# Kernel optimization log

Hardware: AMD Instinct MI355X
Metric: run time of the kernel (lower is better)

The kernel has to match this reference:

```python
import jax, jax.numpy as jnp
import numpy as np

AUX_LOSS_ALPHA = 0.01
TOP_K = 2
N_EXPERTS = 64


def setup_inputs() -> dict:
    key = jax.random.key(0)
    k1, k2 = jax.random.split(key)
    B, S, H, E = 4, 4096, 2048, N_EXPERTS
    hidden_states = jax.random.normal(k1, (B, S, H), dtype=jnp.float32)
    # kaiming_uniform_(a=sqrt(5)) ~ U(-1/sqrt(H), 1/sqrt(H))
    bound = 1.0 / np.sqrt(H)
    weight = jax.random.uniform(k2, (E, H), dtype=jnp.float32, minval=-bound, maxval=bound)
    return {"hidden_states": hidden_states, "weight": weight}


def reference(hidden_states, weight):
    B, S, H = hidden_states.shape
    E, K = N_EXPERTS, TOP_K
    x = hidden_states.reshape(-1, H)              # [T, H], T = B*S
    logits = jnp.einsum('th,eh->te', x, weight)   # router GEMM [T, E]
    scores = jax.nn.softmax(logits, axis=-1)
    topk_weight, topk_idx = jax.lax.top_k(scores, K)  # [T, K]
    # norm_topk_prob (K > 1)
    topk_weight = topk_weight / (jnp.sum(topk_weight, axis=-1, keepdims=True) + 1e-20)
    # seq_aux auxiliary loss (training path)
    idx2d = topk_idx.reshape(B, S * K)            # [B, S*K]
    ce = jnp.zeros((B, E), dtype=scores.dtype)
    ce = ce.at[jnp.arange(B)[:, None], idx2d].add(1.0)
    ce = ce / (S * K / E)
    scores3 = scores.reshape(B, S, E)
    aux_loss = jnp.mean(jnp.sum(ce * jnp.mean(scores3, axis=1), axis=1)) * AUX_LOSS_ALPHA
    return topk_idx, topk_weight, aux_loss
```

## Files before the change

kernel.cpp:

```cpp
#include <hip/hip_runtime.h>
#include <math.h>


#define TT 16384
#define HH 2048
#define EE 64
#define BB 4
#define M_TOK 16
#define KCH 256
#define TAU 2e-3f
#define NREP 8

typedef float v4f __attribute__((ext_vector_type(4)));
typedef float f4v __attribute__((ext_vector_type(4)));
typedef short s8v __attribute__((ext_vector_type(8)));

__device__ __forceinline__ unsigned short f2bf(float f) {
    unsigned u = __float_as_uint(f);
    return (unsigned short)((u + 0x7fffu + ((u >> 16) & 1u)) >> 16);
}
__device__ __forceinline__ float bf2f(unsigned short h) {
    return __uint_as_float(((unsigned)h) << 16);
}

__global__ void prep_b(const float* __restrict__ w,
                       unsigned short* __restrict__ bhi,
                       unsigned short* __restrict__ blo) {
    int idx = blockIdx.x * blockDim.x + threadIdx.x;
    int j    = idx & 7;
    int lane = (idx >> 3) & 63;
    int ks   = (idx >> 9) & 63;
    int nt   = idx >> 15;
    int e = nt * 16 + (lane & 15);
    int k = ks * 32 + (lane >> 4) * 8 + j;
    float f = w[e * HH + k];
    unsigned short h = f2bf(f);
    bhi[idx] = h;
    blo[idx] = f2bf(f - bf2f(h));
}

__global__ __launch_bounds__(256) void gemm_logits(
    const float* __restrict__ x,
    const unsigned short* __restrict__ bhi, const unsigned short* __restrict__ blo,
    float* __restrict__ logits) {

    __shared__ unsigned short ahi[2][8 * 64 * 8];
    __shared__ unsigned short alo[2][8 * 64 * 8];

    const int tid  = threadIdx.x;
    const int wave = tid >> 6;
    const int lane = tid & 63;
    const int tok0 = blockIdx.x * M_TOK;
    const int m  = tid >> 4;
    const int kb = tid & 15;

    v4f rx[2][4];

    auto LD = [&](int c, int s) {
        const float* __restrict__ xp = x + (size_t)(tok0 + m) * HH + c * KCH + kb * 8;
        rx[s][0] = *(const v4f*)xp;
        rx[s][1] = *(const v4f*)(xp + 4);
        rx[s][2] = *(const v4f*)(xp + 128);
        rx[s][3] = *(const v4f*)(xp + 132);
    };
    auto ST = [&](int s, int bi) {
#pragma unroll
        for (int g = 0; g < 2; ++g) {
            v4f a = rx[s][g * 2], b2 = rx[s][g * 2 + 1];
            float xs[8] = {a.x, a.y, a.z, a.w, b2.x, b2.y, b2.z, b2.w};
            s8v hv, lv;
#pragma unroll
            for (int j = 0; j < 8; ++j) {
                unsigned short h = f2bf(xs[j]);
                hv[j] = (short)h;
                lv[j] = (short)f2bf(xs[j] - bf2f(h));
            }
            const int k8i = kb + g * 16;
            const int kstep = k8i >> 2, quad = k8i & 3;
            const int entry = kstep * 64 + quad * 16 + (m ^ (quad << 1));
            *(s8v*)&ahi[bi][entry * 8] = hv;
            *(s8v*)&alo[bi][entry * 8] = lv;
        }
    };

    LD(0, 0);
    LD(1, 1);
    ST(0, 0);
    __syncthreads();

    f4v acc = {0.f, 0.f, 0.f, 0.f};
    const int rdl = lane ^ ((lane >> 4) << 1);

#pragma unroll
    for (int c = 0; c < 8; ++c) {
        const int cur = c & 1;
        if (c < 6) LD(c + 2, cur);
        if (c < 7) ST(cur ^ 1, cur ^ 1);
#pragma unroll
        for (int ks = 0; ks < 8; ++ks) {
            const int entry = ks * 64 + rdl;
            s8v af_h = *(const s8v*)&ahi[cur][entry * 8];
            s8v af_l = *(const s8v*)&alo[cur][entry * 8];
            const size_t boff = ((size_t)(wave * 64 + c * 8 + ks) * 64 + lane) * 8;
            s8v bf_h = *(const s8v*)&bhi[boff];
            s8v bf_l = *(const s8v*)&blo[boff];
            acc = __builtin_amdgcn_mfma_f32_16x16x32_bf16(af_h, bf_h, acc, 0, 0, 0);
            acc = __builtin_amdgcn_mfma_f32_16x16x32_bf16(af_h, bf_l, acc, 0, 0, 0);
            acc = __builtin_amdgcn_mfma_f32_16x16x32_bf16(af_l, bf_h, acc, 0, 0, 0);
        }
        __syncthreads();
    }

#pragma unroll
    for (int r = 0; r < 4; ++r)
        logits[(size_t)(tok0 + (lane >> 4) * 4 + r) * EE + wave * 16 + (lane & 15)] = acc[r];
}

__global__ __launch_bounds__(256) void gate_topk(
    const float* __restrict__ logits,
    float* __restrict__ out_idx, float* __restrict__ out_w,
    float* __restrict__ g_cnt, float* __restrict__ g_ssum,
    int* __restrict__ wl_cnt, int* __restrict__ wl) {

    __shared__ float bssum[EE];
    const int tid  = threadIdx.x;
    const int lane = tid & 63;
    const int t    = blockIdx.x * 4 + (tid >> 6);
    const int rep  = (blockIdx.x & (NREP - 1)) * (BB * EE);

    if (tid < EE) bssum[tid] = 0.f;

    float l = logits[(size_t)t * EE + lane];

    float mx = l;
#pragma unroll
    for (int off = 32; off; off >>= 1) mx = fmaxf(mx, __shfl_xor(mx, off, 64));
    float p = __expf(l - mx);
    float Z = p;
#pragma unroll
    for (int off = 32; off; off >>= 1) Z += __shfl_xor(Z, off, 64);
    float s = p / Z;

    float v = l;
    int cand[4]; float cl[4];
#pragma unroll
    for (int r = 0; r < 4; ++r) {
        float bv = v; int bi = lane;
#pragma unroll
        for (int off = 32; off; off >>= 1) {
            float ov = __shfl_xor(bv, off, 64);
            int   oi = __shfl_xor(bi, off, 64);
            if (ov > bv || (ov == bv && oi < bi)) { bv = ov; bi = oi; }
        }
        cand[r] = bi; cl[r] = bv;
        if (lane == bi) v = -3.4e38f;
    }

    __syncthreads();
    atomicAdd(&bssum[lane], s);

    if (lane == 0) {
        const int b = t >> 12;
        atomicAdd(&g_cnt[rep + b * EE + cand[0]], 1.f);
        atomicAdd(&g_cnt[rep + b * EE + cand[1]], 1.f);
        float w1 = 1.f / (1.f + __expf(cl[1] - cl[0]));
        out_idx[t * 2]     = (float)cand[0];
        out_idx[t * 2 + 1] = (float)cand[1];
        out_w[t * 2]       = w1;
        out_w[t * 2 + 1]   = 1.f - w1;
        if (cl[0] - cl[1] < TAU || cl[1] - cl[2] < TAU) {
            int pos = atomicAdd(wl_cnt, 1);
            wl[pos] = t;
        }
    }

    __syncthreads();
    if (tid < EE) {
        const int b0 = (blockIdx.x * 4) >> 12;
        atomicAdd(&g_ssum[rep + b0 * EE + tid], bssum[tid]);
    }
}

__global__ __launch_bounds__(256) void rerank_exact(
    const float* __restrict__ logits, const float* __restrict__ x,
    const float* __restrict__ w,
    const int* __restrict__ wl_cnt, const int* __restrict__ wl,
    float* __restrict__ out_idx, float* __restrict__ out_w) {

    const int lane = threadIdx.x & 63;
    const int wid  = blockIdx.x * 4 + (threadIdx.x >> 6);
    const int n    = wl_cnt[0];

    for (int i = wid; i < n; i += 32 * 4) {
        const int t = wl[i];
        float l = logits[(size_t)t * EE + lane];

        float v = l;
        int cand[4];
#pragma unroll
        for (int r = 0; r < 4; ++r) {
            float bv = v; int bi = lane;
#pragma unroll
            for (int off = 32; off; off >>= 1) {
                float ov = __shfl_xor(bv, off, 64);
                int   oi = __shfl_xor(bi, off, 64);
                if (ov > bv || (ov == bv && oi < bi)) { bv = ov; bi = oi; }
            }
            cand[r] = bi;
            if (lane == bi) v = -3.4e38f;
        }

        const float* __restrict__ xt  = x + (size_t)t * HH;
        const float* __restrict__ w0p = w + (size_t)cand[0] * HH;
        const float* __restrict__ w1p = w + (size_t)cand[1] * HH;
        const float* __restrict__ w2p = w + (size_t)cand[2] * HH;
        const float* __restrict__ w3p = w + (size_t)cand[3] * HH;
        double d0 = 0.0, d1 = 0.0, d2 = 0.0, d3 = 0.0;
#pragma unroll
        for (int ii = 0; ii < 8; ++ii) {
            const int k = ii * 256 + lane * 4;
            v4f xv = *(const v4f*)(xt + k);
            v4f a0 = *(const v4f*)(w0p + k);
            v4f a1 = *(const v4f*)(w1p + k);
            v4f a2 = *(const v4f*)(w2p + k);
            v4f a3 = *(const v4f*)(w3p + k);
            double dx0 = (double)xv.x, dx1 = (double)xv.y;
            double dx2 = (double)xv.z, dx3 = (double)xv.w;
            d0 = fma(dx0, (double)a0.x, d0); d0 = fma(dx1, (double)a0.y, d0);
            d0 = fma(dx2, (double)a0.z, d0); d0 = fma(dx3, (double)a0.w, d0);
            d1 = fma(dx0, (double)a1.x, d1); d1 = fma(dx1, (double)a1.y, d1);
            d1 = fma(dx2, (double)a1.z, d1); d1 = fma(dx3, (double)a1.w, d1);
            d2 = fma(dx0, (double)a2.x, d2); d2 = fma(dx1, (double)a2.y, d2);
            d2 = fma(dx2, (double)a2.z, d2); d2 = fma(dx3, (double)a2.w, d2);
            d3 = fma(dx0, (double)a3.x, d3); d3 = fma(dx1, (double)a3.y, d3);
            d3 = fma(dx2, (double)a3.z, d3); d3 = fma(dx3, (double)a3.w, d3);
        }
#pragma unroll
        for (int off = 32; off; off >>= 1) {
            d0 += __shfl_xor(d0, off, 64);
            d1 += __shfl_xor(d1, off, 64);
            d2 += __shfl_xor(d2, off, 64);
            d3 += __shfl_xor(d3, off, 64);
        }

        double bd[4] = {d0, d1, d2, d3};
        int e1 = cand[0]; double l1 = bd[0];
#pragma unroll
        for (int r = 1; r < 4; ++r)
            if (bd[r] > l1 || (bd[r] == l1 && cand[r] < e1)) { l1 = bd[r]; e1 = cand[r]; }
        int e2 = -1; double l2 = -1e300;
#pragma unroll
        for (int r = 0; r < 4; ++r) {
            if (cand[r] == e1) continue;
            if (e2 < 0 || bd[r] > l2 || (bd[r] == l2 && cand[r] < e2)) { l2 = bd[r]; e2 = cand[r]; }
        }

        double w1 = 1.0 / (1.0 + exp(l2 - l1));
        if (lane == 0) {
            out_idx[t * 2]     = (float)e1;
            out_idx[t * 2 + 1] = (float)e2;
            out_w[t * 2]       = (float)w1;
            out_w[t * 2 + 1]   = (float)(1.0 - w1);
        }
    }
}

__global__ void finalize(const float* __restrict__ g_cnt,
                         const float* __restrict__ g_ssum,
                         float* __restrict__ aux_out) {
    int lane = threadIdx.x;
    float a = 0.f;
    for (int b = 0; b < BB; ++b) {
        float c = 0.f, ss = 0.f;
#pragma unroll
        for (int r = 0; r < NREP; ++r) {
            c  += g_cnt[r * (BB * EE) + b * EE + lane];
            ss += g_ssum[r * (BB * EE) + b * EE + lane];
        }
        a += c * ss;
    }
#pragma unroll
    for (int off = 32; off; off >>= 1) a += __shfl_xor(a, off, 64);
    if (lane == 0) aux_out[0] = a * (0.01f / (4.f * 128.f * 4096.f));
}

extern "C" void kernel_launch(void* const* d_in, const int* in_sizes, int n_in,
                              void* d_out, int out_size, void* d_ws, size_t ws_size,
                              hipStream_t stream) {
    const float* x = (const float*)d_in[0];
    const float* w = (const float*)d_in[1];
    float* out = (float*)d_out;
    float* out_idx = out;
    float* out_w   = out + 2 * TT;
    float* aux     = out + 4 * TT;

    float* logits = (float*)d_ws;
    unsigned short* bhi = (unsigned short*)(logits + (size_t)TT * EE);
    unsigned short* blo = bhi + (size_t)EE * HH;
    float* g_cnt  = (float*)(blo + (size_t)EE * HH);
    float* g_ssum = g_cnt + NREP * BB * EE;
    int*   wl_cnt = (int*)(g_ssum + NREP * BB * EE);
    int*   wl     = wl_cnt + 16;

    hipMemsetAsync(g_cnt, 0, (2 * NREP * BB * EE + 16) * sizeof(float), stream);
    prep_b<<<(EE * HH) / 256, 256, 0, stream>>>(w, bhi, blo);
    gemm_logits<<<TT / M_TOK, 256, 0, stream>>>(x, bhi, blo, logits);
    gate_topk<<<TT / 4, 256, 0, stream>>>(logits, out_idx, out_w,
                                          g_cnt, g_ssum, wl_cnt, wl);
    rerank_exact<<<32, 256, 0, stream>>>(logits, x, w, wl_cnt, wl, out_idx, out_w);
    finalize<<<1, 64, 0, stream>>>(g_cnt, g_ssum, aux);
}
```

Before: 245.9 us.

## Process 32 tokens per GEMM block to reuse weight fragments across two tiles

Doubles the token tile per block in the router GEMM so each bf16 hi/lo weight fragment loaded from global memory feeds two MFMA accumulators, halving weight traffic. The LDS double buffer is replaced by a single buffer written after a barrier, with register prefetch of the next chunk. This trades load/compute overlap and grid size (half as many blocks) for less redundant weight reads.

```diff
diff --git a/kernel.cpp b/kernel.cpp
--- a/kernel.cpp
+++ b/kernel.cpp
@@ -6,7 +6,7 @@
 #define HH 2048
 #define EE 64
 #define BB 4
-#define M_TOK 16
+#define M_TOK 32
 #define KCH 256
 #define TAU 2e-3f
 #define NREP 8
@@ -44,8 +44,8 @@
     const unsigned short* __restrict__ bhi, const unsigned short* __restrict__ blo,
     float* __restrict__ logits) {
 
-    __shared__ unsigned short ahi[2][8 * 64 * 8];
-    __shared__ unsigned short alo[2][8 * 64 * 8];
+    __shared__ unsigned short ahi[2 * 8 * 64 * 8];
+    __shared__ unsigned short alo[2 * 8 * 64 * 8];
 
     const int tid  = threadIdx.x;
     const int wave = tid >> 6;
@@ -56,64 +56,86 @@
 
     v4f rx[2][4];
 
-    auto LD = [&](int c, int s) {
-        const float* __restrict__ xp = x + (size_t)(tok0 + m) * HH + c * KCH + kb * 8;
-        rx[s][0] = *(const v4f*)xp;
-        rx[s][1] = *(const v4f*)(xp + 4);
-        rx[s][2] = *(const v4f*)(xp + 128);
-        rx[s][3] = *(const v4f*)(xp + 132);
+    auto LD = [&](int c) {
+#pragma unroll
+        for (int mt = 0; mt < 2; ++mt) {
+            const float* __restrict__ xp =
+                x + (size_t)(tok0 + mt * 16 + m) * HH + c * KCH + kb * 8;
+            rx[mt][0] = *(const v4f*)xp;
+            rx[mt][1] = *(const v4f*)(xp + 4);
+            rx[mt][2] = *(const v4f*)(xp + 128);
+            rx[mt][3] = *(const v4f*)(xp + 132);
+        }
     };
-    auto ST = [&](int s, int bi) {
-#pragma unroll
-        for (int g = 0; g < 2; ++g) {
-            v4f a = rx[s][g * 2], b2 = rx[s][g * 2 + 1];
-            float xs[8] = {a.x, a.y, a.z, a.w, b2.x, b2.y, b2.z, b2.w};
-            s8v hv, lv;
-#pragma unroll
-            for (int j = 0; j < 8; ++j) {
-                unsigned short h = f2bf(xs[j]);
-                hv[j] = (short)h;
-                lv[j] = (short)f2bf(xs[j] - bf2f(h));
+    auto ST = [&]() {
+#pragma unroll
+        for (int mt = 0; mt < 2; ++mt) {
+#pragma unroll
+            for (int g = 0; g < 2; ++g) {
+                v4f a = rx[mt][g * 2], b2 = rx[mt][g * 2 + 1];
+                float xs[8] = {a.x, a.y, a.z, a.w, b2.x, b2.y, b2.z, b2.w};
+                s8v hv, lv;
+#pragma unroll
+                for (int j = 0; j < 8; ++j) {
+                    unsigned short h = f2bf(xs[j]);
+                    hv[j] = (short)h;
+                    lv[j] = (short)f2bf(xs[j] - bf2f(h));
+                }
+                const int k8i = kb + g * 16;
+                const int ks = k8i >> 2, quad = k8i & 3;
+                const int entry = (mt * 8 + ks) * 64 + quad * 16 + (m ^ (quad << 1));
+                *(s8v*)&ahi[entry * 8] = hv;
+                *(s8v*)&alo[entry * 8] = lv;
             }
-            const int k8i = kb + g * 16;
-            const int kstep = k8i >> 2, quad = k8i & 3;
-            const int entry = kstep * 64 + quad * 16 + (m ^ (quad << 1));
-            *(s8v*)&ahi[bi][entry * 8] = hv;
-            *(s8v*)&alo[bi][entry * 8] = lv;
         }
     };
 
-    LD(0, 0);
-    LD(1, 1);
-    ST(0, 0);
+    LD(0);
+    ST();
     __syncthreads();
 
-    f4v acc = {0.f, 0.f, 0.f, 0.f};
+    f4v acc0 = {0.f, 0.f, 0.f, 0.f};
+    f4v acc1 = {0.f, 0.f, 0.f, 0.f};
     const int rdl = lane ^ ((lane >> 4) << 1);
 
-#pragma unroll
     for (int c = 0; c < 8; ++c) {
-        const int cur = c & 1;
-        if (c < 6) LD(c + 2, cur);
-        if (c < 7) ST(cur ^ 1, cur ^ 1);
+        if (c < 7) LD(c + 1);
 #pragma unroll
         for (int ks = 0; ks < 8; ++ks) {
-            const int entry = ks * 64 + rdl;
-            s8v af_h = *(const s8v*)&ahi[cur][entry * 8];
-            s8v af_l = *(const s8v*)&alo[cur][entry * 8];
             const size_t boff = ((size_t)(wave * 64 + c * 8 + ks) * 64 + lane) * 8;
             s8v bf_h = *(const s8v*)&bhi[boff];
             s8v bf_l = *(const s8v*)&blo[boff];
-            acc = __builtin_amdgcn_mfma_f32_16x16x32_bf16(af_h, bf_h, acc, 0, 0, 0);
-            acc = __builtin_amdgcn_mfma_f32_16x16x32_bf16(af_h, bf_l, acc, 0, 0, 0);
-            acc = __builtin_amdgcn_mfma_f32_16x16x32_bf16(af_l, bf_h, acc, 0, 0, 0);
+            {
+                const int entry = ks * 64 + rdl;
+                s8v af_h = *(const s8v*)&ahi[entry * 8];
+                s8v af_l = *(const s8v*)&alo[entry * 8];
+                acc0 = __builtin_amdgcn_mfma_f32_16x16x32_bf16(af_h, bf_h, acc0, 0, 0, 0);
+                acc0 = __builtin_amdgcn_mfma_f32_16x16x32_bf16(af_h, bf_l, acc0, 0, 0, 0);
+                acc0 = __builtin_amdgcn_mfma_f32_16x16x32_bf16(af_l, bf_h, acc0, 0, 0, 0);
+            }
+            {
+                const int entry = (8 + ks) * 64 + rdl;
+                s8v af_h = *(const s8v*)&ahi[entry * 8];
+                s8v af_l = *(const s8v*)&alo[entry * 8];
+                acc1 = __builtin_amdgcn_mfma_f32_16x16x32_bf16(af_h, bf_h, acc1, 0, 0, 0);
+                acc1 = __builtin_amdgcn_mfma_f32_16x16x32_bf16(af_h, bf_l, acc1, 0, 0, 0);
+                acc1 = __builtin_amdgcn_mfma_f32_16x16x32_bf16(af_l, bf_h, acc1, 0, 0, 0);
+            }
         }
         __syncthreads();
-    }
-
-#pragma unroll
-    for (int r = 0; r < 4; ++r)
-        logits[(size_t)(tok0 + (lane >> 4) * 4 + r) * EE + wave * 16 + (lane & 15)] = acc[r];
+        if (c < 7) {
+            ST();
+            __syncthreads();
+        }
+    }
+
+#pragma unroll
+    for (int r = 0; r < 4; ++r) {
+        const int row = (lane >> 4) * 4 + r;
+        const int col = wave * 16 + (lane & 15);
+        logits[(size_t)(tok0 + row) * EE + col]      = acc0[r];
+        logits[(size_t)(tok0 + 16 + row) * EE + col] = acc1[r];
+    }
 }
 
 __global__ __launch_bounds__(256) void gate_topk(
```

After: 254.0 us. +3.3%, slower.

## Split GEMM over K across waves, drop LDS staging, reduce partials in gate kernel

Applied to the files above, without the earlier changes.

The router GEMM now gives each wave a quarter of the hidden dimension for all 64 experts. Each wave loads its x fragment straight from global memory into registers, converts it to bf16 hi/lo there, and prefetches the next k-step, so the LDS staging and __syncthreads are gone. Each x element is converted to bf16 once, where before it was converted per chunk into shared memory. The four partial logit planes are written to workspace and summed in gate_topk and rerank_exact. This trades barrier overhead for four times the logit write and read traffic (about 16 MB extra each way) and higher register use.

```diff
diff --git a/kernel.cpp b/kernel.cpp
--- a/kernel.cpp
+++ b/kernel.cpp
@@ -6,8 +6,6 @@
 #define HH 2048
 #define EE 64
 #define BB 4
-#define M_TOK 16
-#define KCH 256
 #define TAU 2e-3f
 #define NREP 8
 
@@ -39,85 +37,78 @@
     blo[idx] = f2bf(f - bf2f(h));
 }
 
-__global__ __launch_bounds__(256) void gemm_logits(
+__global__ __launch_bounds__(256, 4) void gemm_partial(
     const float* __restrict__ x,
     const unsigned short* __restrict__ bhi, const unsigned short* __restrict__ blo,
-    float* __restrict__ logits) {
-
-    __shared__ unsigned short ahi[2][8 * 64 * 8];
-    __shared__ unsigned short alo[2][8 * 64 * 8];
+    float* __restrict__ plog) {
 
     const int tid  = threadIdx.x;
-    const int wave = tid >> 6;
+    const int kseg = tid >> 6;
     const int lane = tid & 63;
-    const int tok0 = blockIdx.x * M_TOK;
-    const int m  = tid >> 4;
-    const int kb = tid & 15;
-
-    v4f rx[2][4];
-
-    auto LD = [&](int c, int s) {
-        const float* __restrict__ xp = x + (size_t)(tok0 + m) * HH + c * KCH + kb * 8;
-        rx[s][0] = *(const v4f*)xp;
-        rx[s][1] = *(const v4f*)(xp + 4);
-        rx[s][2] = *(const v4f*)(xp + 128);
-        rx[s][3] = *(const v4f*)(xp + 132);
-    };
-    auto ST = [&](int s, int bi) {
-#pragma unroll
-        for (int g = 0; g < 2; ++g) {
-            v4f a = rx[s][g * 2], b2 = rx[s][g * 2 + 1];
-            float xs[8] = {a.x, a.y, a.z, a.w, b2.x, b2.y, b2.z, b2.w};
-            s8v hv, lv;
-#pragma unroll
-            for (int j = 0; j < 8; ++j) {
-                unsigned short h = f2bf(xs[j]);
-                hv[j] = (short)h;
-                lv[j] = (short)f2bf(xs[j] - bf2f(h));
+    const int tok0 = blockIdx.x * 16;
+
+    const float* __restrict__ xr =
+        x + (size_t)(tok0 + (lane & 15)) * HH + kseg * 512 + (lane >> 4) * 8;
+    const int ks0 = kseg * 16;
+
+    f4v acc[4];
+#pragma unroll
+    for (int nt = 0; nt < 4; ++nt) acc[nt] = (f4v){0.f, 0.f, 0.f, 0.f};
+
+    v4f a0 = *(const v4f*)xr;
+    v4f a1 = *(const v4f*)(xr + 4);
+    s8v bh[4], bl[4];
+#pragma unroll
+    for (int nt = 0; nt < 4; ++nt) {
+        const size_t off = ((size_t)(nt * 64 + ks0) * 64 + lane) * 8;
+        bh[nt] = *(const s8v*)&bhi[off];
+        bl[nt] = *(const s8v*)&blo[off];
+    }
+
+#pragma unroll
+    for (int ks = 0; ks < 16; ++ks) {
+        v4f na0, na1;
+        s8v nbh[4], nbl[4];
+        if (ks < 15) {
+            na0 = *(const v4f*)(xr + (ks + 1) * 32);
+            na1 = *(const v4f*)(xr + (ks + 1) * 32 + 4);
+#pragma unroll
+            for (int nt = 0; nt < 4; ++nt) {
+                const size_t off = ((size_t)(nt * 64 + ks0 + ks + 1) * 64 + lane) * 8;
+                nbh[nt] = *(const s8v*)&bhi[off];
+                nbl[nt] = *(const s8v*)&blo[off];
             }
-            const int k8i = kb + g * 16;
-            const int kstep = k8i >> 2, quad = k8i & 3;
-            const int entry = kstep * 64 + quad * 16 + (m ^ (quad << 1));
-            *(s8v*)&ahi[bi][entry * 8] = hv;
-            *(s8v*)&alo[bi][entry * 8] = lv;
-        }
-    };
-
-    LD(0, 0);
-    LD(1, 1);
-    ST(0, 0);
-    __syncthreads();
-
-    f4v acc = {0.f, 0.f, 0.f, 0.f};
-    const int rdl = lane ^ ((lane >> 4) << 1);
-
-#pragma unroll
-    for (int c = 0; c < 8; ++c) {
-        const int cur = c & 1;
-        if (c < 6) LD(c + 2, cur);
-        if (c < 7) ST(cur ^ 1, cur ^ 1);
-#pragma unroll
-        for (int ks = 0; ks < 8; ++ks) {
-            const int entry = ks * 64 + rdl;
-            s8v af_h = *(const s8v*)&ahi[cur][entry * 8];
-            s8v af_l = *(const s8v*)&alo[cur][entry * 8];
-            const size_t boff = ((size_t)(wave * 64 + c * 8 + ks) * 64 + lane) * 8;
-            s8v bf_h = *(const s8v*)&bhi[boff];
-            s8v bf_l = *(const s8v*)&blo[boff];
-            acc = __builtin_amdgcn_mfma_f32_16x16x32_bf16(af_h, bf_h, acc, 0, 0, 0);
-            acc = __builtin_amdgcn_mfma_f32_16x16x32_bf16(af_h, bf_l, acc, 0, 0, 0);
-            acc = __builtin_amdgcn_mfma_f32_16x16x32_bf16(af_l, bf_h, acc, 0, 0, 0);
-        }
-        __syncthreads();
-    }
-
-#pragma unroll
-    for (int r = 0; r < 4; ++r)
-        logits[(size_t)(tok0 + (lane >> 4) * 4 + r) * EE + wave * 16 + (lane & 15)] = acc[r];
+        }
+        float xs[8] = {a0.x, a0.y, a0.z, a0.w, a1.x, a1.y, a1.z, a1.w};
+        s8v ah, al;
+#pragma unroll
+        for (int j = 0; j < 8; ++j) {
+            unsigned short h = f2bf(xs[j]);
+            ah[j] = (short)h;
+            al[j] = (short)f2bf(xs[j] - bf2f(h));
+        }
+#pragma unroll
+        for (int nt = 0; nt < 4; ++nt) {
+            acc[nt] = __builtin_amdgcn_mfma_f32_16x16x32_bf16(ah, bh[nt], acc[nt], 0, 0, 0);
+            acc[nt] = __builtin_amdgcn_mfma_f32_16x16x32_bf16(ah, bl[nt], acc[nt], 0, 0, 0);
+            acc[nt] = __builtin_amdgcn_mfma_f32_16x16x32_bf16(al, bh[nt], acc[nt], 0, 0, 0);
+        }
+        a0 = na0; a1 = na1;
+#pragma unroll
+        for (int nt = 0; nt < 4; ++nt) { bh[nt] = nbh[nt]; bl[nt] = nbl[nt]; }
+    }
+
+    float* __restrict__ pout = plog + (size_t)kseg * TT * EE;
+#pragma unroll
+    for (int nt = 0; nt < 4; ++nt)
+#pragma unroll
+        for (int r = 0; r < 4; ++r)
+            pout[(size_t)(tok0 + (lane >> 4) * 4 + r) * EE + nt * 16 + (lane & 15)] =
+                acc[nt][r];
 }
 
 __global__ __launch_bounds__(256) void gate_topk(
-    const float* __restrict__ logits,
+    const float* __restrict__ plog,
     float* __restrict__ out_idx, float* __restrict__ out_w,
     float* __restrict__ g_cnt, float* __restrict__ g_ssum,
     int* __restrict__ wl_cnt, int* __restrict__ wl) {
@@ -130,7 +121,9 @@
 
     if (tid < EE) bssum[tid] = 0.f;
 
-    float l = logits[(size_t)t * EE + lane];
+    const size_t o = (size_t)t * EE + lane;
+    float l = plog[o] + plog[(size_t)TT * EE + o] +
+              plog[2 * (size_t)TT * EE + o] + plog[3 * (size_t)TT * EE + o];
 
     float mx = l;
 #pragma unroll
@@ -182,7 +175,7 @@
 }
 
 __global__ __launch_bounds__(256) void rerank_exact(
-    const float* __restrict__ logits, const float* __restrict__ x,
+    const float* __restrict__ plog, const float* __restrict__ x,
     const float* __restrict__ w,
     const int* __restrict__ wl_cnt, const int* __restrict__ wl,
     float* __restrict__ out_idx, float* __restrict__ out_w) {
@@ -193,7 +186,9 @@
 
     for (int i = wid; i < n; i += 32 * 4) {
         const int t = wl[i];
-        float l = logits[(size_t)t * EE + lane];
+        const size_t o = (size_t)t * EE + lane;
+        float l = plog[o] + plog[(size_t)TT * EE + o] +
+                  plog[2 * (size_t)TT * EE + o] + plog[3 * (size_t)TT * EE + o];
 
         float v = l;
         int cand[4];
@@ -294,8 +289,8 @@
     float* out_w   = out + 2 * TT;
     float* aux     = out + 4 * TT;
 
-    float* logits = (float*)d_ws;
-    unsigned short* bhi = (unsigned short*)(logits + (size_t)TT * EE);
+    float* plog = (float*)d_ws;
+    unsigned short* bhi = (unsigned short*)(plog + 4 * (size_t)TT * EE);
     unsigned short* blo = bhi + (size_t)EE * HH;
     float* g_cnt  = (float*)(blo + (size_t)EE * HH);
     float* g_ssum = g_cnt + NREP * BB * EE;
@@ -304,9 +299,9 @@
 
     hipMemsetAsync(g_cnt, 0, (2 * NREP * BB * EE + 16) * sizeof(float), stream);
     prep_b<<<(EE * HH) / 256, 256, 0, stream>>>(w, bhi, blo);
-    gemm_logits<<<TT / M_TOK, 256, 0, stream>>>(x, bhi, blo, logits);
-    gate_topk<<<TT / 4, 256, 0, stream>>>(logits, out_idx, out_w,
+    gemm_partial<<<TT / 16, 256, 0, stream>>>(x, bhi, blo, plog);
+    gate_topk<<<TT / 4, 256, 0, stream>>>(plog, out_idx, out_w,
                                           g_cnt, g_ssum, wl_cnt, wl);
-    rerank_exact<<<32, 256, 0, stream>>>(logits, x, w, wl_cnt, wl, out_idx, out_w);
+    rerank_exact<<<32, 256, 0, stream>>>(plog, x, w, wl_cnt, wl, out_idx, out_w);
     finalize<<<1, 64, 0, stream>>>(g_cnt, g_ssum, aux);
 }
```

Measured after the change: 254.2 us. 3.4% more time.
